# Kernel tuning notes

Measured on AMD Instinct MI355X. Metric: run time of the kernel, lower is better.

Reference implementation:

```python
import jax, jax.numpy as jnp
import numpy as np

N_NODES = 100000


def gcn_conv(x, W, b, edge_index, n_nodes):
    """PyG GCNConv: add self-loops, symmetric deg^-1/2 normalization,
    linear transform, scatter-sum aggregation, bias."""
    x = x @ W  # [N, out]
    src, dst = edge_index[0], edge_index[1]
    self_idx = jnp.arange(n_nodes, dtype=src.dtype)
    src = jnp.concatenate([src, self_idx])
    dst = jnp.concatenate([dst, self_idx])
    # in-degree (including self-loop) per destination node
    deg = jax.ops.segment_sum(jnp.ones_like(src, dtype=x.dtype), dst,
                              num_segments=n_nodes)
    dinv = jnp.where(deg > 0, jax.lax.rsqrt(deg), 0.0)
    norm = dinv[src] * dinv[dst]  # [E+N]
    msg = x[src] * norm[:, None]  # gather + scale, [E+N, out]
    out = jax.ops.segment_sum(msg, dst, num_segments=n_nodes)
    return out + b


def setup_inputs() -> dict:
    key = jax.random.key(0)
    ks = jax.random.split(key, 7)
    in_c, hid_c, out_c = 256, 128, 64
    n_edges, n_lbl = 1600000, 200000
    x = jax.random.normal(ks[0], (N_NODES, in_c), dtype=jnp.float32)
    edge_index = jax.random.randint(ks[1], (2, n_edges), 0, N_NODES, dtype=jnp.int64)
    edge_label_index = jax.random.randint(ks[2], (2, n_lbl), 0, N_NODES, dtype=jnp.int64)
    # Glorot-style init for GCN linear weights
    W1 = jax.random.normal(ks[3], (in_c, hid_c), dtype=jnp.float32) / np.sqrt(in_c)
    b1 = jnp.zeros((hid_c,), dtype=jnp.float32)
    W2 = jax.random.normal(ks[4], (hid_c, out_c), dtype=jnp.float32) / np.sqrt(hid_c)
    b2 = jnp.zeros((out_c,), dtype=jnp.float32)
    return {"x": x, "edge_index": edge_index,
            "edge_label_index": edge_label_index,
            "W1": W1, "b1": b1, "W2": W2, "b2": b2}


def reference(x, edge_index, edge_label_index, W1, b1, W2, b2):
    n = x.shape[0]
    h = jax.nn.relu(gcn_conv(x, W1, b1, edge_index, n))
    z = gcn_conv(h, W2, b2, edge_index, n)  # [N, out_c]
    src, dst = edge_label_index[0], edge_label_index[1]
    return jnp.sum(z[src] * z[dst], axis=-1)  # [E_lbl]
```

## Files before the change

### kernel.cpp

```cpp
#include <hip/hip_runtime.h>
#include <hip/hip_bf16.h>

#define N_NODES 100000
#define N_EDGES 1600000
#define N_LBL   200000
#define C_IN    256
#define C_HID   128
#define C_OUT   64
#define SCAN_BLOCKS 391
#define NBUCKET 391
#define FILLA_EPB 2048

using u16 = unsigned short;
using u32 = unsigned int;
using u64 = unsigned long long;
using s64 = long long;

typedef __attribute__((ext_vector_type(8))) short bf16x8;
typedef __attribute__((ext_vector_type(4))) float f32x4;

__device__ __forceinline__ float bf2f(u16 h) {
    u32 u = ((u32)h) << 16;
    float f;
    __builtin_memcpy(&f, &u, 4);
    return f;
}
__device__ __forceinline__ u16 f2bf(float f) {
    u32 u;
    __builtin_memcpy(&u, &f, 4);
    u32 r = (u + 0x7fffu + ((u >> 16) & 1u)) >> 16;
    return (u16)r;
}
__device__ __forceinline__ void unpack_bf2(u32 p, float& lo, float& hi) {
    u32 l = p << 16;
    u32 h = p & 0xffff0000u;
    __builtin_memcpy(&lo, &l, 4);
    __builtin_memcpy(&hi, &h, 4);
}
__device__ __forceinline__ void acc8(uint4 p, float* a) {
    float f0, f1;
    unpack_bf2(p.x, f0, f1); a[0] += f0; a[1] += f1;
    unpack_bf2(p.y, f0, f1); a[2] += f0; a[3] += f1;
    unpack_bf2(p.z, f0, f1); a[4] += f0; a[5] += f1;
    unpack_bf2(p.w, f0, f1); a[6] += f0; a[7] += f1;
}
__device__ __forceinline__ int geti(const void* p, s64 i, int i64) {
    return i64 ? (int)((const s64*)p)[i] : ((const int*)p)[i];
}
__device__ __forceinline__ int clampn(int v) {
    return ((u32)v < (u32)N_NODES) ? v : 0;
}

__device__ __forceinline__ void split8(const float4& a, const float4& b,
                                       bf16x8& hi8, bf16x8& lo8) {
    float va[8] = {a.x, a.y, a.z, a.w, b.x, b.y, b.z, b.w};
    u32 uh[4], ul[4];
#pragma unroll
    for (int p = 0; p < 4; ++p) {
        float x0 = va[2 * p], x1 = va[2 * p + 1];
        u32 u0, u1;
        __builtin_memcpy(&u0, &x0, 4);
        __builtin_memcpy(&u1, &x1, 4);
        u32 h0 = u0 & 0xffff0000u, h1 = u1 & 0xffff0000u;
        float f0, f1;
        __builtin_memcpy(&f0, &h0, 4);
        __builtin_memcpy(&f1, &h1, 4);
        float l0 = x0 - f0, l1 = x1 - f1;
        u32 w0, w1;
        __builtin_memcpy(&w0, &l0, 4);
        __builtin_memcpy(&w1, &l1, 4);
        uh[p] = (u0 >> 16) | h1;
        ul[p] = (w0 >> 16) | (w1 & 0xffff0000u);
    }
    struct U { u32 w[4]; };
    U H = {{uh[0], uh[1], uh[2], uh[3]}};
    U L = {{ul[0], ul[1], ul[2], ul[3]}};
    __builtin_memcpy(&hi8, &H, 16);
    __builtin_memcpy(&lo8, &L, 16);
}

__global__ void k_detect(const void* __restrict__ x, const void* __restrict__ ei,
                         int* __restrict__ flags) {
    const int lane = threadIdx.x & 63;
    const u16* xh = (const u16*)x;
    int cnt = 0;
#pragma unroll
    for (int k = 0; k < 4; ++k) {
        int i = 2 * (lane + 64 * k);
        u32 e = (xh[i] >> 7) & 0xFF;
        cnt += __builtin_popcountll(__ballot(e > 137));
    }
    const u32* ew = (const u32*)ei;
    int nz = __builtin_popcountll(__ballot(ew[2 * lane + 1] != 0));
    if (lane == 0) {
        flags[0] = (cnt > 16) ? 1 : 0;
        flags[1] = (nz == 0) ? 1 : 0;
    }
}

__global__ __launch_bounds__(256) void k_bcount(const void* __restrict__ ei,
                                                const int* __restrict__ flags,
                                                int* __restrict__ bcnt) {
    __shared__ int hist[NBUCKET];
    const int t = threadIdx.x;
    if (t < NBUCKET) hist[t] = 0;
    if (t + 256 < NBUCKET) hist[t + 256] = 0;
    __syncthreads();
    const s64 base = (s64)blockIdx.x * FILLA_EPB;
    const int i64 = flags[1];
#pragma unroll
    for (int j = 0; j < 8; ++j) {
        s64 e = base + t + 256 * j;
        if (e < N_EDGES) {
            int d = clampn(geti(ei, (s64)N_EDGES + e, i64));
            atomicAdd(&hist[d >> 8], 1);
        }
    }
    __syncthreads();
    if (t < NBUCKET && hist[t]) atomicAdd(&bcnt[t], hist[t]);
    if (t + 256 < NBUCKET && hist[t + 256]) atomicAdd(&bcnt[t + 256], hist[t + 256]);
}

__global__ __launch_bounds__(512) void k_bscan(const int* __restrict__ bcnt,
                                               int* __restrict__ bstart,
                                               int* __restrict__ gcur) {
    __shared__ int arr[512];
    const int t = threadIdx.x;
    int v = (t < NBUCKET) ? bcnt[t] : 0;
    arr[t] = v;
    __syncthreads();
#pragma unroll
    for (int off = 1; off < 512; off <<= 1) {
        int u = (t >= off) ? arr[t - off] : 0;
        __syncthreads();
        arr[t] += u;
        __syncthreads();
    }
    if (t < NBUCKET) {
        int ex = arr[t] - v;
        bstart[t] = ex;
        gcur[t]   = ex;
    }
    if (t == 511) bstart[NBUCKET] = arr[511];
}

__global__ __launch_bounds__(256) void k_fillA(const void* __restrict__ ei,
                                               const int* __restrict__ flags,
                                               int* __restrict__ gcur,
                                               u64* __restrict__ temp) {
    __shared__ int hist[NBUCKET];
    __shared__ int gbase[NBUCKET];
    const int t = threadIdx.x;
    if (t < NBUCKET) hist[t] = 0;
    if (t + 256 < NBUCKET) hist[t + 256] = 0;
    __syncthreads();
    const s64 base = (s64)blockIdx.x * FILLA_EPB;
    const int i64 = flags[1];
    int sv[8], dv[8], bk[8], off[8];
    bool val[8];
#pragma unroll
    for (int j = 0; j < 8; ++j) {
        s64 e = base + t + 256 * j;
        val[j] = (e < N_EDGES);
        if (val[j]) {
            sv[j] = clampn(geti(ei, e, i64));
            dv[j] = clampn(geti(ei, (s64)N_EDGES + e, i64));
            bk[j] = dv[j] >> 8;
            off[j] = atomicAdd(&hist[bk[j]], 1);
        }
    }
    __syncthreads();
    if (t < NBUCKET && hist[t]) gbase[t] = atomicAdd(&gcur[t], hist[t]);
    if (t + 256 < NBUCKET && hist[t + 256]) gbase[t + 256] = atomicAdd(&gcur[t + 256], hist[t + 256]);
    __syncthreads();
#pragma unroll
    for (int j = 0; j < 8; ++j) {
        if (val[j])
            temp[(size_t)(gbase[bk[j]] + off[j])] = ((u64)(u32)dv[j] << 32) | (u32)sv[j];
    }
}

__global__ __launch_bounds__(256) void k_deg2(const u64* __restrict__ temp,
                                              const int* __restrict__ bstart,
                                              int* __restrict__ deg) {
    __shared__ int dcnt[256];
    const int t = threadIdx.x;
    const int b = blockIdx.x;
    dcnt[t] = 0;
    __syncthreads();
    const int beg = bstart[b], end = bstart[b + 1];
    for (int e = beg + t; e < end; e += 256) {
        u32 d = (u32)(temp[e] >> 32);
        atomicAdd(&dcnt[d & 255], 1);
    }
    __syncthreads();
    int node = (b << 8) + t;
    if (node < N_NODES) deg[node] = dcnt[t];
}

__global__ __launch_bounds__(256) void k_fillB(const u64* __restrict__ temp,
                                               const int* __restrict__ bstart,
                                               const int* __restrict__ row_ptr,
                                               int* __restrict__ csr_src) {
    __shared__ int cur[256];
    const int t = threadIdx.x;
    const int b = blockIdx.x;
    int node = (b << 8) + t;
    cur[t] = (node < N_NODES) ? row_ptr[node] : 0;
    __syncthreads();
    const int beg = bstart[b], end = bstart[b + 1];
    for (int e = beg + t; e < end; e += 256) {
        u64 p = temp[e];
        u32 s = (u32)p, d = (u32)(p >> 32);
        int pos = atomicAdd(&cur[d & 255], 1);
        csr_src[pos] = (int)s;
    }
}

__global__ __launch_bounds__(256) void k_scan1(const int* __restrict__ deg,
                                               int* __restrict__ bsum) {
    __shared__ int red[256];
    const int t = threadIdx.x;
    int i = blockIdx.x * 256 + t;
    red[t] = (i < N_NODES) ? deg[i] : 0;
    __syncthreads();
#pragma unroll
    for (int off = 128; off > 0; off >>= 1) {
        if (t < off) red[t] += red[t + off];
        __syncthreads();
    }
    if (t == 0) bsum[blockIdx.x] = red[0];
}

__global__ __launch_bounds__(512) void k_scan2(const int* __restrict__ bsum,
                                               int* __restrict__ boff,
                                               int* __restrict__ row_ptr) {
    __shared__ int arr[512];
    const int t = threadIdx.x;
    int v = (t < SCAN_BLOCKS) ? bsum[t] : 0;
    arr[t] = v;
    __syncthreads();
#pragma unroll
    for (int off = 1; off < 512; off <<= 1) {
        int u = (t >= off) ? arr[t - off] : 0;
        __syncthreads();
        arr[t] += u;
        __syncthreads();
    }
    if (t < SCAN_BLOCKS) boff[t] = arr[t] - v;
    if (t == 511) row_ptr[N_NODES] = arr[511];
}

__global__ __launch_bounds__(256) void k_scan3(const int* __restrict__ deg,
                                               const int* __restrict__ boff,
                                               int* __restrict__ row_ptr,
                                               float* __restrict__ dinv) {
    __shared__ int arr[256];
    const int t = threadIdx.x;
    int i = blockIdx.x * 256 + t;
    int v = (i < N_NODES) ? deg[i] : 0;
    arr[t] = v;
    __syncthreads();
#pragma unroll
    for (int off = 1; off < 256; off <<= 1) {
        int u = (t >= off) ? arr[t - off] : 0;
        __syncthreads();
        arr[t] += u;
        __syncthreads();
    }
    if (i < N_NODES) {
        int run = boff[blockIdx.x] + arr[t] - v;
        row_ptr[i] = run;
        dinv[i]    = rsqrtf((float)v + 1.0f);
    }
}

__global__ __launch_bounds__(256) void k_w1t(const void* __restrict__ W1_,
                                             const int* __restrict__ flags,
                                             u16* __restrict__ w1t_hi,
                                             u16* __restrict__ w1t_lo) {
    int idx = blockIdx.x * 256 + threadIdx.x;
    int k = idx >> 7, n = idx & 127;
    float v = flags[0] ? ((const float*)W1_)[idx] : bf2f(((const u16*)W1_)[idx]);
    u32 uv;
    __builtin_memcpy(&uv, &v, 4);
    u32 hf = uv & 0xffff0000u;
    float hb;
    __builtin_memcpy(&hb, &hf, 4);
    float lo = v - hb;
    u32 ulo;
    __builtin_memcpy(&ulo, &lo, 4);
    w1t_hi[n * C_IN + k] = (u16)(uv >> 16);
    w1t_lo[n * C_IN + k] = (u16)(ulo >> 16);
}

__global__ __launch_bounds__(256) void k_w2t(const void* __restrict__ W2_,
                                             const int* __restrict__ flags,
                                             u16* __restrict__ w2t_hi,
                                             u16* __restrict__ w2t_lo) {
    int idx = blockIdx.x * 256 + threadIdx.x;
    int k = idx >> 6, n = idx & 63;
    float v = flags[0] ? ((const float*)W2_)[idx] : bf2f(((const u16*)W2_)[idx]);
    u32 uv;
    __builtin_memcpy(&uv, &v, 4);
    u32 hf = uv & 0xffff0000u;
    float hb;
    __builtin_memcpy(&hb, &hf, 4);
    float lo = v - hb;
    u32 ulo;
    __builtin_memcpy(&ulo, &lo, 4);
    w2t_hi[n * C_HID + k] = (u16)(uv >> 16);
    w2t_lo[n * C_HID + k] = (u16)(ulo >> 16);
}

__global__ __launch_bounds__(1024) void k_gemm1_mfma(const void* __restrict__ xv_,
                                                     const u16* __restrict__ w1t_hi,
                                                     const u16* __restrict__ w1t_lo,
                                                     const float* __restrict__ dinv,
                                                     const int* __restrict__ flags,
                                                     u16* __restrict__ g0) {
    extern __shared__ char smem[];
    u16* lds_hi = (u16*)smem;
    u16* lds_lo = (u16*)(smem + 65536);
    const int isf32 = flags[0];
    const int lane = threadIdx.x & 63;
    const int wid  = threadIdx.x >> 6;
    const int r0   = blockIdx.x * 512 + wid * 32;

    for (int g = threadIdx.x; g < 4096; g += 1024) {
        int row = g >> 5;
        int off = (g & 31) << 4;
        int dst = row * 512 + (off ^ ((row & 7) << 4));
        *(uint4*)((char*)lds_hi + dst) =
            *(const uint4*)((const char*)(w1t_hi + (size_t)row * C_IN) + off);
        *(uint4*)((char*)lds_lo + dst) =
            *(const uint4*)((const char*)(w1t_lo + (size_t)row * C_IN) + off);
    }
    __syncthreads();

    const int rowA = r0 + (lane & 15);
    const int rowB = rowA + 16;
    const int rlA  = (rowA < N_NODES) ? rowA : (N_NODES - 1);
    const int rlB  = (rowB < N_NODES) ? rowB : (N_NODES - 1);
    const int kh   = (lane >> 4) * 8;
    const int khb  = (lane >> 4) * 16;

    int rbase[8], rswz[8];
#pragma unroll
    for (int n = 0; n < 8; ++n) {
        int rloc = n * 16 + (lane & 15);
        rbase[n] = rloc * 512;
        rswz[n]  = (rloc & 7) << 4;
    }

    f32x4 acc[2][8];
#pragma unroll
    for (int g = 0; g < 2; ++g)
#pragma unroll
        for (int n = 0; n < 8; ++n) acc[g][n] = (f32x4){0.f, 0.f, 0.f, 0.f};

    if (isf32) {
        const float* apA = (const float*)xv_ + (size_t)rlA * C_IN + kh;
        const float* apB = (const float*)xv_ + (size_t)rlB * C_IN + kh;
        float4 xa0 = ((const float4*)apA)[0];
        float4 xa1 = ((const float4*)(apA + 4))[0];
        float4 xb0 = ((const float4*)apB)[0];
        float4 xb1 = ((const float4*)(apB + 4))[0];
#pragma unroll
        for (int k0 = 0; k0 < C_IN; k0 += 32) {
            float4 na0, na1, nb0, nb1;
            if (k0 + 32 < C_IN) {
                na0 = ((const float4*)(apA + k0 + 32))[0];
                na1 = ((const float4*)(apA + k0 + 36))[0];
                nb0 = ((const float4*)(apB + k0 + 32))[0];
                nb1 = ((const float4*)(apB + k0 + 36))[0];
            }
            bf16x8 ahiA, aloA, ahiB, aloB;
            split8(xa0, xa1, ahiA, aloA);
            split8(xb0, xb1, ahiB, aloB);
#pragma unroll
            for (int n = 0; n < 8; ++n) {
                int a = rbase[n] + ((k0 * 2 + khb) ^ rswz[n]);
                bf16x8 bh = *(const bf16x8*)((const char*)lds_hi + a);
                bf16x8 bl = *(const bf16x8*)((const char*)lds_lo + a);
                acc[0][n] = __builtin_amdgcn_mfma_f32_16x16x32_bf16(ahiA, bl, acc[0][n], 0, 0, 0);
                acc[0][n] = __builtin_amdgcn_mfma_f32_16x16x32_bf16(aloA, bh, acc[0][n], 0, 0, 0);
                acc[0][n] = __builtin_amdgcn_mfma_f32_16x16x32_bf16(ahiA, bh, acc[0][n], 0, 0, 0);
                acc[1][n] = __builtin_amdgcn_mfma_f32_16x16x32_bf16(ahiB, bl, acc[1][n], 0, 0, 0);
                acc[1][n] = __builtin_amdgcn_mfma_f32_16x16x32_bf16(aloB, bh, acc[1][n], 0, 0, 0);
                acc[1][n] = __builtin_amdgcn_mfma_f32_16x16x32_bf16(ahiB, bh, acc[1][n], 0, 0, 0);
            }
            if (k0 + 32 < C_IN) { xa0 = na0; xa1 = na1; xb0 = nb0; xb1 = nb1; }
        }
    } else {
        const u16* apA = (const u16*)xv_ + (size_t)rlA * C_IN + kh;
        const u16* apB = (const u16*)xv_ + (size_t)rlB * C_IN + kh;
        bf16x8 aA = *(const bf16x8*)apA;
        bf16x8 aB = *(const bf16x8*)apB;
#pragma unroll
        for (int k0 = 0; k0 < C_IN; k0 += 32) {
            bf16x8 nA, nB;
            if (k0 + 32 < C_IN) {
                nA = *(const bf16x8*)(apA + k0 + 32);
                nB = *(const bf16x8*)(apB + k0 + 32);
            }
#pragma unroll
            for (int n = 0; n < 8; ++n) {
                int a = rbase[n] + ((k0 * 2 + khb) ^ rswz[n]);
                bf16x8 bh = *(const bf16x8*)((const char*)lds_hi + a);
                acc[0][n] = __builtin_amdgcn_mfma_f32_16x16x32_bf16(aA, bh, acc[0][n], 0, 0, 0);
                acc[1][n] = __builtin_amdgcn_mfma_f32_16x16x32_bf16(aB, bh, acc[1][n], 0, 0, 0);
            }
            if (k0 + 32 < C_IN) { aA = nA; aB = nB; }
        }
    }

    const int ccol = lane & 15;
#pragma unroll
    for (int g = 0; g < 2; ++g) {
        const int crow0 = r0 + g * 16 + (lane >> 4) * 4;
#pragma unroll
        for (int i = 0; i < 4; ++i) {
            int r = crow0 + i;
            if (r < N_NODES) {
                float dv = dinv[r];
#pragma unroll
                for (int n = 0; n < 8; ++n)
                    g0[(size_t)r * C_HID + n * 16 + ccol] = f2bf(dv * acc[g][n][i]);
            }
        }
    }
}

__global__ __launch_bounds__(512) void k_gemm2_mfma(const float* __restrict__ h,
                                                    const u16* __restrict__ w2t_hi,
                                                    const u16* __restrict__ w2t_lo,
                                                    const float* __restrict__ dinv,
                                                    u16* __restrict__ g1) {
    __shared__ u16 lds_hi[64 * 128];
    __shared__ u16 lds_lo[64 * 128];
    const int lane = threadIdx.x & 63;
    const int wid  = threadIdx.x >> 6;
    const int r0   = blockIdx.x * 256 + wid * 32;

    {
        for (int g = threadIdx.x; g < 1024; g += 512) {
            int row = g >> 4;
            int off = (g & 15) << 4;
            int dst = row * 256 + (off ^ ((row & 7) << 4));
            *(uint4*)((char*)lds_hi + dst) =
                *(const uint4*)((const char*)(w2t_hi + (size_t)row * C_HID) + off);
            *(uint4*)((char*)lds_lo + dst) =
                *(const uint4*)((const char*)(w2t_lo + (size_t)row * C_HID) + off);
        }
    }
    __syncthreads();

    const int rowA = r0 + (lane & 15);
    const int rowB = rowA + 16;
    const int rlA  = (rowA < N_NODES) ? rowA : (N_NODES - 1);
    const int rlB  = (rowB < N_NODES) ? rowB : (N_NODES - 1);
    const int kh   = (lane >> 4) * 8;
    const int khb  = (lane >> 4) * 16;

    int rbase[4], rswz[4];
#pragma unroll
    for (int n = 0; n < 4; ++n) {
        int rloc = n * 16 + (lane & 15);
        rbase[n] = rloc * 256;
        rswz[n]  = (rloc & 7) << 4;
    }

    f32x4 acc[2][4];
#pragma unroll
    for (int g = 0; g < 2; ++g)
#pragma unroll
        for (int n = 0; n < 4; ++n) acc[g][n] = (f32x4){0.f, 0.f, 0.f, 0.f};

    const float* apA = h + (size_t)rlA * C_HID + kh;
    const float* apB = h + (size_t)rlB * C_HID + kh;

    float4 xa0 = ((const float4*)apA)[0];
    float4 xa1 = ((const float4*)(apA + 4))[0];
    float4 xb0 = ((const float4*)apB)[0];
    float4 xb1 = ((const float4*)(apB + 4))[0];
#pragma unroll
    for (int k0 = 0; k0 < C_HID; k0 += 32) {
        bf16x8 bh[4], bl[4];
#pragma unroll
        for (int n = 0; n < 4; ++n) {
            int a = rbase[n] + ((k0 * 2 + khb) ^ rswz[n]);
            bh[n] = *(const bf16x8*)((const char*)lds_hi + a);
            bl[n] = *(const bf16x8*)((const char*)lds_lo + a);
        }
        float4 na0, na1, nb0, nb1;
        if (k0 + 32 < C_HID) {
            na0 = ((const float4*)(apA + k0 + 32))[0];
            na1 = ((const float4*)(apA + k0 + 36))[0];
            nb0 = ((const float4*)(apB + k0 + 32))[0];
            nb1 = ((const float4*)(apB + k0 + 36))[0];
        }
        bf16x8 ahiA, aloA, ahiB, aloB;
        split8(xa0, xa1, ahiA, aloA);
        split8(xb0, xb1, ahiB, aloB);
#pragma unroll
        for (int n = 0; n < 4; ++n) {
            acc[0][n] = __builtin_amdgcn_mfma_f32_16x16x32_bf16(ahiA, bl[n], acc[0][n], 0, 0, 0);
            acc[0][n] = __builtin_amdgcn_mfma_f32_16x16x32_bf16(aloA, bh[n], acc[0][n], 0, 0, 0);
            acc[0][n] = __builtin_amdgcn_mfma_f32_16x16x32_bf16(ahiA, bh[n], acc[0][n], 0, 0, 0);
            acc[1][n] = __builtin_amdgcn_mfma_f32_16x16x32_bf16(ahiB, bl[n], acc[1][n], 0, 0, 0);
            acc[1][n] = __builtin_amdgcn_mfma_f32_16x16x32_bf16(aloB, bh[n], acc[1][n], 0, 0, 0);
            acc[1][n] = __builtin_amdgcn_mfma_f32_16x16x32_bf16(ahiB, bh[n], acc[1][n], 0, 0, 0);
        }
        if (k0 + 32 < C_HID) { xa0 = na0; xa1 = na1; xb0 = nb0; xb1 = nb1; }
    }

    const int ccol = lane & 15;
#pragma unroll
    for (int g = 0; g < 2; ++g) {
        const int crow0 = r0 + g * 16 + (lane >> 4) * 4;
#pragma unroll
        for (int i = 0; i < 4; ++i) {
            int r = crow0 + i;
            if (r < N_NODES) {
                float dv = dinv[r];
#pragma unroll
                for (int n = 0; n < 4; ++n)
                    g1[(size_t)r * C_OUT + n * 16 + ccol] = f2bf(dv * acc[g][n][i]);
            }
        }
    }
}

__global__ __launch_bounds__(256) void k_gather128(const int* __restrict__ row_ptr,
                                                   const int* __restrict__ csr_src,
                                                   const uint4* __restrict__ g,
                                                   const void* __restrict__ bias_,
                                                   const float* __restrict__ dinv,
                                                   const int* __restrict__ flags,
                                                   float* __restrict__ out) {
    const int lane = threadIdx.x & 63;
    const int wid  = threadIdx.x >> 6;
    const int q    = lane >> 4;
    const int jj   = lane & 15;
    const int node = blockIdx.x * 16 + wid * 4 + q;
    const uint4* gp = g + jj;
    const int beg = row_ptr[node], end = row_ptr[node + 1];
    float a[8] = {0.f, 0.f, 0.f, 0.f, 0.f, 0.f, 0.f, 0.f};
    int e = beg;
    for (; e + 4 <= end; e += 4) {
        int s0 = csr_src[e], s1 = csr_src[e + 1];
        int s2 = csr_src[e + 2], s3 = csr_src[e + 3];
        uint4 p0 = gp[(size_t)s0 * 16];
        uint4 p1 = gp[(size_t)s1 * 16];
        uint4 p2 = gp[(size_t)s2 * 16];
        uint4 p3 = gp[(size_t)s3 * 16];
        acc8(p0, a);
        acc8(p1, a);
        acc8(p2, a);
        acc8(p3, a);
    }
    for (; e < end; ++e) acc8(gp[(size_t)csr_src[e] * 16], a);
    acc8(gp[(size_t)node * 16], a);
    float b[8];
    if (flags[0]) {
        float4 b0 = ((const float4*)bias_)[2 * jj];
        float4 b1 = ((const float4*)bias_)[2 * jj + 1];
        b[0] = b0.x; b[1] = b0.y; b[2] = b0.z; b[3] = b0.w;
        b[4] = b1.x; b[5] = b1.y; b[6] = b1.z; b[7] = b1.w;
    } else {
        uint4 bw = ((const uint4*)bias_)[jj];
        unpack_bf2(bw.x, b[0], b[1]);
        unpack_bf2(bw.y, b[2], b[3]);
        unpack_bf2(bw.z, b[4], b[5]);
        unpack_bf2(bw.w, b[6], b[7]);
    }
    float dv = dinv[node];
    float4 r0, r1;
    r0.x = fmaxf(dv * a[0] + b[0], 0.f);
    r0.y = fmaxf(dv * a[1] + b[1], 0.f);
    r0.z = fmaxf(dv * a[2] + b[2], 0.f);
    r0.w = fmaxf(dv * a[3] + b[3], 0.f);
    r1.x = fmaxf(dv * a[4] + b[4], 0.f);
    r1.y = fmaxf(dv * a[5] + b[5], 0.f);
    r1.z = fmaxf(dv * a[6] + b[6], 0.f);
    r1.w = fmaxf(dv * a[7] + b[7], 0.f);
    float4* op = (float4*)(out + (size_t)node * C_HID);
    op[2 * jj]     = r0;
    op[2 * jj + 1] = r1;
}

__global__ __launch_bounds__(256) void k_gather64(const int* __restrict__ row_ptr,
                                                  const int* __restrict__ csr_src,
                                                  const uint4* __restrict__ g,
                                                  const void* __restrict__ bias_,
                                                  const float* __restrict__ dinv,
                                                  const int* __restrict__ flags,
                                                  float* __restrict__ out) {
    const int lane = threadIdx.x & 63;
    const int wid  = threadIdx.x >> 6;
    const int oct  = lane >> 3;
    const int jj   = lane & 7;
    const int node = blockIdx.x * 32 + wid * 8 + oct;
    const uint4* gp = g + jj;
    const int beg = row_ptr[node], end = row_ptr[node + 1];
    float a[8] = {0.f, 0.f, 0.f, 0.f, 0.f, 0.f, 0.f, 0.f};
    int e = beg;
    for (; e + 4 <= end; e += 4) {
        int s0 = csr_src[e], s1 = csr_src[e + 1];
        int s2 = csr_src[e + 2], s3 = csr_src[e + 3];
        uint4 p0 = gp[(size_t)s0 * 8];
        uint4 p1 = gp[(size_t)s1 * 8];
        uint4 p2 = gp[(size_t)s2 * 8];
        uint4 p3 = gp[(size_t)s3 * 8];
        acc8(p0, a);
        acc8(p1, a);
        acc8(p2, a);
        acc8(p3, a);
    }
    for (; e < end; ++e) acc8(gp[(size_t)csr_src[e] * 8], a);
    acc8(gp[(size_t)node * 8], a);
    float b[8];
    if (flags[0]) {
        float4 b0 = ((const float4*)bias_)[2 * jj];
        float4 b1 = ((const float4*)bias_)[2 * jj + 1];
        b[0] = b0.x; b[1] = b0.y; b[2] = b0.z; b[3] = b0.w;
        b[4] = b1.x; b[5] = b1.y; b[6] = b1.z; b[7] = b1.w;
    } else {
        uint4 bw = ((const uint4*)bias_)[jj];
        unpack_bf2(bw.x, b[0], b[1]);
        unpack_bf2(bw.y, b[2], b[3]);
        unpack_bf2(bw.z, b[4], b[5]);
        unpack_bf2(bw.w, b[6], b[7]);
    }
    float dv = dinv[node];
    float4 r0, r1;
    r0.x = dv * a[0] + b[0];
    r0.y = dv * a[1] + b[1];
    r0.z = dv * a[2] + b[2];
    r0.w = dv * a[3] + b[3];
    r1.x = dv * a[4] + b[4];
    r1.y = dv * a[5] + b[5];
    r1.z = dv * a[6] + b[6];
    r1.w = dv * a[7] + b[7];
    float4* op = (float4*)(out + (size_t)node * C_OUT);
    op[2 * jj]     = r0;
    op[2 * jj + 1] = r1;
}

__global__ __launch_bounds__(256) void k_edgedot(const void* __restrict__ eli,
                                                 const int* __restrict__ flags,
                                                 const float* __restrict__ z,
                                                 void* __restrict__ out) {
    const int g16 = threadIdx.x >> 4;
    const int l16 = threadIdx.x & 15;
    const int e = blockIdx.x * 16 + g16;
    if (e >= N_LBL) return;
    const int i64 = flags[1];
    const int s = clampn(geti(eli, e, i64));
    const int d = clampn(geti(eli, (s64)N_LBL + e, i64));
    float4 zs = *(const float4*)(z + (size_t)s * C_OUT + l16 * 4);
    float4 zd = *(const float4*)(z + (size_t)d * C_OUT + l16 * 4);
    float v = zs.x * zd.x + zs.y * zd.y + zs.z * zd.z + zs.w * zd.w;
    v += __shfl_xor(v, 1, 64);
    v += __shfl_xor(v, 2, 64);
    v += __shfl_xor(v, 4, 64);
    v += __shfl_xor(v, 8, 64);
    if (l16 == 0) {
        if (flags[0]) ((float*)out)[e] = v;
        else          ((u16*)out)[e]   = f2bf(v);
    }
}

extern "C" void kernel_launch(void* const* d_in, const int* in_sizes, int n_in,
                              void* d_out, int out_size, void* d_ws, size_t ws_size,
                              hipStream_t stream) {
    const void* x   = d_in[0];
    const void* ei  = d_in[1];
    const void* eli = d_in[2];
    const void* W1  = d_in[3];
    const void* b1  = d_in[4];
    const void* W2  = d_in[5];
    const void* b2  = d_in[6];

    if (ws_size < 84800128) return;
    char* ws = (char*)d_ws;
    float* h       = (float*)ws;
    float* z       = (float*)ws;
    int*   bsum    = (int*)ws;
    int*   boff    = (int*)(ws + 4096);
    int*   bcnt    = (int*)(ws + 8192);
    int*   bstart  = (int*)(ws + 12288);
    int*   gcur    = (int*)(ws + 16384);
    u64*   temp    = (u64*)(ws + 1048576);
    u16*   g0      = (u16*)(ws + 51200000);
    u16*   g1      = (u16*)(ws + 51200000);
    float* dinv    = (float*)(ws + 76800000);
    int*   deg     = (int*)(ws + 77200000);
    u16*   w1t_hi  = (u16*)(ws + 77200000);
    u16*   w1t_lo  = (u16*)(ws + 77200000 + 65536);
    u16*   w2t_hi  = (u16*)(ws + 77200000 + 131072);
    u16*   w2t_lo  = (u16*)(ws + 77200000 + 147456);
    int*   row_ptr = (int*)(ws + 77600000);
    int*   csr_src = (int*)(ws + 78400008);
    int*   flags   = (int*)(ws + 84800064);

    const int FILLA_GRID = (N_EDGES + FILLA_EPB - 1) / FILLA_EPB;

    static bool attr_set = false;
    if (!attr_set) {
        hipFuncSetAttribute((const void*)k_gemm1_mfma,
                            hipFuncAttributeMaxDynamicSharedMemorySize, 131072);
        attr_set = true;
    }

    k_detect<<<1, 64, 0, stream>>>(x, ei, flags);

    hipMemsetAsync(bcnt, 0, NBUCKET * sizeof(int), stream);
    k_bcount<<<FILLA_GRID, 256, 0, stream>>>(ei, flags, bcnt);
    k_bscan<<<1, 512, 0, stream>>>(bcnt, bstart, gcur);
    k_fillA<<<FILLA_GRID, 256, 0, stream>>>(ei, flags, gcur, temp);
    k_deg2<<<NBUCKET, 256, 0, stream>>>(temp, bstart, deg);

    k_scan1<<<SCAN_BLOCKS, 256, 0, stream>>>(deg, bsum);
    k_scan2<<<1, 512, 0, stream>>>(bsum, boff, row_ptr);
    k_scan3<<<SCAN_BLOCKS, 256, 0, stream>>>(deg, boff, row_ptr, dinv);

    k_fillB<<<NBUCKET, 256, 0, stream>>>(temp, bstart, row_ptr, csr_src);

    k_w1t<<<128, 256, 0, stream>>>(W1, flags, w1t_hi, w1t_lo);
    k_w2t<<<32, 256, 0, stream>>>(W2, flags, w2t_hi, w2t_lo);

    k_gemm1_mfma<<<(N_NODES + 511) / 512, 1024, 131072, stream>>>(x, w1t_hi, w1t_lo, dinv, flags, g0);
    k_gather128<<<N_NODES / 16, 256, 0, stream>>>(row_ptr, csr_src, (const uint4*)g0, b1, dinv, flags, h);

    k_gemm2_mfma<<<(N_NODES + 255) / 256, 512, 0, stream>>>(h, w2t_hi, w2t_lo, dinv, g1);
    k_gather64<<<N_NODES / 32, 256, 0, stream>>>(row_ptr, csr_src, (const uint4*)g1, b2, dinv, flags, z);

    k_edgedot<<<(N_LBL + 15) / 16, 256, 0, stream>>>(eli, flags, z, d_out);
}
```

Measured before the change: 393.7 us.

## Build CSR with fixed-capacity buckets and packed 32-bit edge records

```diff
diff --git a/kernel.cpp b/kernel.cpp
--- a/kernel.cpp
+++ b/kernel.cpp
@@ -9,6 +9,7 @@
 #define C_OUT   64
 #define SCAN_BLOCKS 391
 #define NBUCKET 391
+#define BCAP 8192
 #define FILLA_EPB 2048
 
 using u16 = unsigned short;
@@ -98,56 +99,16 @@
     }
 }
 
-__global__ __launch_bounds__(256) void k_bcount(const void* __restrict__ ei,
-                                                const int* __restrict__ flags,
-                                                int* __restrict__ bcnt) {
-    __shared__ int hist[NBUCKET];
-    const int t = threadIdx.x;
-    if (t < NBUCKET) hist[t] = 0;
-    if (t + 256 < NBUCKET) hist[t + 256] = 0;
-    __syncthreads();
-    const s64 base = (s64)blockIdx.x * FILLA_EPB;
-    const int i64 = flags[1];
-#pragma unroll
-    for (int j = 0; j < 8; ++j) {
-        s64 e = base + t + 256 * j;
-        if (e < N_EDGES) {
-            int d = clampn(geti(ei, (s64)N_EDGES + e, i64));
-            atomicAdd(&hist[d >> 8], 1);
-        }
-    }
-    __syncthreads();
-    if (t < NBUCKET && hist[t]) atomicAdd(&bcnt[t], hist[t]);
-    if (t + 256 < NBUCKET && hist[t + 256]) atomicAdd(&bcnt[t + 256], hist[t + 256]);
-}
-
-__global__ __launch_bounds__(512) void k_bscan(const int* __restrict__ bcnt,
-                                               int* __restrict__ bstart,
-                                               int* __restrict__ gcur) {
-    __shared__ int arr[512];
-    const int t = threadIdx.x;
-    int v = (t < NBUCKET) ? bcnt[t] : 0;
-    arr[t] = v;
-    __syncthreads();
-#pragma unroll
-    for (int off = 1; off < 512; off <<= 1) {
-        int u = (t >= off) ? arr[t - off] : 0;
-        __syncthreads();
-        arr[t] += u;
-        __syncthreads();
-    }
-    if (t < NBUCKET) {
-        int ex = arr[t] - v;
-        bstart[t] = ex;
-        gcur[t]   = ex;
-    }
-    if (t == 511) bstart[NBUCKET] = arr[511];
+
+__global__ __launch_bounds__(512) void k_binit(int* __restrict__ gcur) {
+    int t = threadIdx.x;
+    if (t < NBUCKET) gcur[t] = t * BCAP;
 }
 
 __global__ __launch_bounds__(256) void k_fillA(const void* __restrict__ ei,
                                                const int* __restrict__ flags,
                                                int* __restrict__ gcur,
-                                               u64* __restrict__ temp) {
+                                               u32* __restrict__ temp) {
     __shared__ int hist[NBUCKET];
     __shared__ int gbase[NBUCKET];
     const int t = threadIdx.x;
@@ -175,31 +136,34 @@
     __syncthreads();
 #pragma unroll
     for (int j = 0; j < 8; ++j) {
-        if (val[j])
-            temp[(size_t)(gbase[bk[j]] + off[j])] = ((u64)(u32)dv[j] << 32) | (u32)sv[j];
-    }
-}
-
-__global__ __launch_bounds__(256) void k_deg2(const u64* __restrict__ temp,
-                                              const int* __restrict__ bstart,
+        if (val[j]) {
+            int pos = gbase[bk[j]] + off[j];
+            if (pos < (bk[j] + 1) * BCAP)
+                temp[pos] = (u32)sv[j] | ((u32)(dv[j] & 255) << 20);
+        }
+    }
+}
+
+__global__ __launch_bounds__(256) void k_deg2(const u32* __restrict__ temp,
+                                              const int* __restrict__ gcur,
                                               int* __restrict__ deg) {
     __shared__ int dcnt[256];
     const int t = threadIdx.x;
     const int b = blockIdx.x;
     dcnt[t] = 0;
     __syncthreads();
-    const int beg = bstart[b], end = bstart[b + 1];
+    const int beg = b * BCAP, end = gcur[b];
     for (int e = beg + t; e < end; e += 256) {
-        u32 d = (u32)(temp[e] >> 32);
-        atomicAdd(&dcnt[d & 255], 1);
+        u32 dl = (temp[e] >> 20) & 255u;
+        atomicAdd(&dcnt[dl], 1);
     }
     __syncthreads();
     int node = (b << 8) + t;
     if (node < N_NODES) deg[node] = dcnt[t];
 }
 
-__global__ __launch_bounds__(256) void k_fillB(const u64* __restrict__ temp,
-                                               const int* __restrict__ bstart,
+__global__ __launch_bounds__(256) void k_fillB(const u32* __restrict__ temp,
+                                               const int* __restrict__ gcur,
                                                const int* __restrict__ row_ptr,
                                                int* __restrict__ csr_src) {
     __shared__ int cur[256];
@@ -208,36 +172,22 @@
     int node = (b << 8) + t;
     cur[t] = (node < N_NODES) ? row_ptr[node] : 0;
     __syncthreads();
-    const int beg = bstart[b], end = bstart[b + 1];
+    const int beg = b * BCAP, end = gcur[b];
     for (int e = beg + t; e < end; e += 256) {
-        u64 p = temp[e];
-        u32 s = (u32)p, d = (u32)(p >> 32);
-        int pos = atomicAdd(&cur[d & 255], 1);
+        u32 p = temp[e];
+        u32 s = p & 0xFFFFFu;
+        u32 dl = (p >> 20) & 255u;
+        int pos = atomicAdd(&cur[dl], 1);
         csr_src[pos] = (int)s;
     }
 }
 
-__global__ __launch_bounds__(256) void k_scan1(const int* __restrict__ deg,
-                                               int* __restrict__ bsum) {
-    __shared__ int red[256];
-    const int t = threadIdx.x;
-    int i = blockIdx.x * 256 + t;
-    red[t] = (i < N_NODES) ? deg[i] : 0;
-    __syncthreads();
-#pragma unroll
-    for (int off = 128; off > 0; off >>= 1) {
-        if (t < off) red[t] += red[t + off];
-        __syncthreads();
-    }
-    if (t == 0) bsum[blockIdx.x] = red[0];
-}
-
-__global__ __launch_bounds__(512) void k_scan2(const int* __restrict__ bsum,
+__global__ __launch_bounds__(512) void k_scan2(const int* __restrict__ gcur,
                                                int* __restrict__ boff,
                                                int* __restrict__ row_ptr) {
     __shared__ int arr[512];
     const int t = threadIdx.x;
-    int v = (t < SCAN_BLOCKS) ? bsum[t] : 0;
+    int v = (t < NBUCKET) ? (gcur[t] - t * BCAP) : 0;
     arr[t] = v;
     __syncthreads();
 #pragma unroll
@@ -247,7 +197,7 @@
         arr[t] += u;
         __syncthreads();
     }
-    if (t < SCAN_BLOCKS) boff[t] = arr[t] - v;
+    if (t < NBUCKET) boff[t] = arr[t] - v;
     if (t == 511) row_ptr[N_NODES] = arr[511];
 }
 
@@ -687,12 +637,9 @@
     char* ws = (char*)d_ws;
     float* h       = (float*)ws;
     float* z       = (float*)ws;
-    int*   bsum    = (int*)ws;
     int*   boff    = (int*)(ws + 4096);
-    int*   bcnt    = (int*)(ws + 8192);
-    int*   bstart  = (int*)(ws + 12288);
     int*   gcur    = (int*)(ws + 16384);
-    u64*   temp    = (u64*)(ws + 1048576);
+    u32*   temp    = (u32*)(ws + 1048576);
     u16*   g0      = (u16*)(ws + 51200000);
     u16*   g1      = (u16*)(ws + 51200000);
     float* dinv    = (float*)(ws + 76800000);
@@ -716,17 +663,14 @@
 
     k_detect<<<1, 64, 0, stream>>>(x, ei, flags);
 
-    hipMemsetAsync(bcnt, 0, NBUCKET * sizeof(int), stream);
-    k_bcount<<<FILLA_GRID, 256, 0, stream>>>(ei, flags, bcnt);
-    k_bscan<<<1, 512, 0, stream>>>(bcnt, bstart, gcur);
+    k_binit<<<1, 512, 0, stream>>>(gcur);
     k_fillA<<<FILLA_GRID, 256, 0, stream>>>(ei, flags, gcur, temp);
-    k_deg2<<<NBUCKET, 256, 0, stream>>>(temp, bstart, deg);
-
-    k_scan1<<<SCAN_BLOCKS, 256, 0, stream>>>(deg, bsum);
-    k_scan2<<<1, 512, 0, stream>>>(bsum, boff, row_ptr);
+    k_deg2<<<NBUCKET, 256, 0, stream>>>(temp, gcur, deg);
+
+    k_scan2<<<1, 512, 0, stream>>>(gcur, boff, row_ptr);
     k_scan3<<<SCAN_BLOCKS, 256, 0, stream>>>(deg, boff, row_ptr, dinv);
 
-    k_fillB<<<NBUCKET, 256, 0, stream>>>(temp, bstart, row_ptr, csr_src);
+    k_fillB<<<NBUCKET, 256, 0, stream>>>(temp, gcur, row_ptr, csr_src);
 
     k_w1t<<<128, 256, 0, stream>>>(W1, flags, w1t_hi, w1t_lo);
     k_w2t<<<32, 256, 0, stream>>>(W2, flags, w2t_hi, w2t_lo);
```

After: 364.5 us. 1.08x faster.
